# Kernel tuning notes

Hardware: AMD Instinct MI355X
Metric: run time of the kernel (lower is better)

The kernel has to match this reference:

```python
import jax, jax.numpy as jnp
import numpy as np

B, S, D, H = 4, 2048, 512, 8
HD = D // H


def rotate_half(t):
    half = t.shape[-1] // 2
    return jnp.concatenate([-t[..., half:], t[..., :half]], axis=-1)


def setup_inputs() -> dict:
    key = jax.random.key(0)
    ks = jax.random.split(key, 8)
    x = jax.random.normal(ks[0], (B, S, D), dtype=jnp.float32)
    # realistic rotary tables built from angles
    inv_freq = 1.0 / (10000.0 ** (jnp.arange(0, D // 2, dtype=jnp.float32) / (D // 2)))
    ang = jnp.arange(S, dtype=jnp.float32)[:, None] * inv_freq[None, :]  # [S, D/2]
    ang = jnp.concatenate([ang, ang], axis=-1)  # [S, D]
    cos_emb = jnp.cos(ang)[None]  # [1, S, D]
    sin_emb = jnp.sin(ang)[None]
    mask = jax.random.randint(ks[1], (B, S, S), 0, 2).astype(jnp.bool_)
    scale = 1.0 / np.sqrt(D)
    wq = jax.random.normal(ks[2], (D, D), dtype=jnp.float32) * scale
    wk = jax.random.normal(ks[3], (D, D), dtype=jnp.float32) * scale
    wv = jax.random.normal(ks[4], (D, D), dtype=jnp.float32) * scale
    wo = jax.random.normal(ks[5], (D, D), dtype=jnp.float32) * scale
    return {"x": x, "cos_emb": cos_emb, "sin_emb": sin_emb, "mask": mask,
            "wq": wq, "wk": wk, "wv": wv, "wo": wo}


def reference(x, cos_emb, sin_emb, mask, wq, wk, wv, wo):
    bsz, seqlen, dim = x.shape
    # projections (weights stored as [in, out])
    xq = x @ wq
    xk = x @ wk
    xv = x @ wv
    # RoPE applied over full dim before head split (as in original)
    xq = xq * cos_emb + rotate_half(xq) * sin_emb
    xk = xk * cos_emb + rotate_half(xk) * sin_emb
    # split heads: [B, H, S, HD]
    xq = xq.reshape(bsz, seqlen, H, HD).transpose(0, 2, 1, 3)
    xk = xk.reshape(bsz, seqlen, H, HD).transpose(0, 2, 1, 3)
    xv = xv.reshape(bsz, seqlen, H, HD).transpose(0, 2, 1, 3)
    scores = jnp.einsum('bhqd,bhkd->bhqk', xq, xk) / jnp.sqrt(jnp.float32(HD))
    scores = scores + (~mask)[:, None].astype(scores.dtype) * (-1e9)
    scores = jax.nn.softmax(scores.astype(jnp.float32), axis=-1).astype(xq.dtype)
    scores = scores * mask[:, None].astype(scores.dtype)
    out = jnp.einsum('bhqk,bhkd->bhqd', scores, xv)
    out = out.transpose(0, 2, 1, 3).reshape(bsz, seqlen, dim)
    return out @ wo
```

## Files before the change

kernel.cpp:

```cpp
#include <hip/hip_runtime.h>
#include <hip/hip_bf16.h>

typedef __bf16 bf16x8 __attribute__((ext_vector_type(8)));
typedef float f32x4 __attribute__((ext_vector_type(4)));
typedef short short8 __attribute__((ext_vector_type(8)));

#define MFMA16(a, b, c) __builtin_amdgcn_mfma_f32_16x16x32_bf16((a), (b), (c), 0, 0, 0)

static constexpr int S = 2048;
static constexpr int D = 512;
static constexpr int HD = 64;
static constexpr int KBLK = 64;
#define QSCALE 0.18033688011112042f

typedef __attribute__((address_space(1))) const unsigned int gu32;
typedef __attribute__((address_space(3))) unsigned int lu32;

__device__ __forceinline__ void gll16(const void* g, void* l) {
  __builtin_amdgcn_global_load_lds((gu32*)g, (lu32*)l, 16, 0, 0);
}

__device__ __forceinline__ unsigned short f2b(float f) {
  return __builtin_bit_cast(unsigned short, __float2bfloat16(f));
}
__device__ __forceinline__ float b2f(unsigned short u) {
  return __builtin_bit_cast(float, (unsigned)u << 16);
}

__global__ void maskbits_kernel(const int* __restrict__ m, unsigned long long* __restrict__ bits) {
  const int stride = 2048 * 256;
  const int lane0 = (threadIdx.x & 63) == 0;
  for (int gid = blockIdx.x * 256 + threadIdx.x; gid < 4 * 2048 * 2048; gid += stride) {
    unsigned long long w = __ballot(m[gid] != 0);
    if (lane0) bits[gid >> 6] = w;
  }
}

__global__ void cast_x_kernel(const float* __restrict__ x, unsigned short* __restrict__ xb) {
  int idx = blockIdx.x * 256 + threadIdx.x;
  float4 v = ((const float4*)x)[idx];
  ushort4 o;
  o.x = f2b(v.x); o.y = f2b(v.y); o.z = f2b(v.z); o.w = f2b(v.w);
  ((ushort4*)xb)[idx] = o;
}

__global__ void wtrans4_kernel(const float* __restrict__ wq, const float* __restrict__ wk,
                               const float* __restrict__ wv, const float* __restrict__ wo,
                               unsigned short* __restrict__ wqkvT, unsigned short* __restrict__ woT) {
  __shared__ float t[64][65];
  const int z = blockIdx.z;
  const float* w = (z == 0) ? wq : (z == 1) ? wk : (z == 2) ? wv : wo;
  unsigned short* dst = (z < 3) ? wqkvT + (size_t)z * 512 * 512 : woT;
  const int i0 = blockIdx.x * 64, o0 = blockIdx.y * 64;
  for (int it = 0; it < 16; ++it) {
    int idx = it * 256 + threadIdx.x;
    int ii = idx >> 6, oo = idx & 63;
    t[oo][ii] = w[(size_t)(i0 + ii) * 512 + o0 + oo];
  }
  __syncthreads();
  for (int it = 0; it < 16; ++it) {
    int idx = it * 256 + threadIdx.x;
    int oo = idx >> 6, ii = idx & 63;
    dst[(size_t)(o0 + oo) * 512 + i0 + ii] = f2b(t[oo][ii]);
  }
}

__global__ __launch_bounds__(256)
void gemm2(const unsigned short* __restrict__ A, const unsigned short* __restrict__ Bt,
           int M, int N, int K, float* __restrict__ Cf,
           unsigned short* __restrict__ qd, unsigned short* __restrict__ kd,
           unsigned short* __restrict__ vtd, int mode) {
  __shared__ alignas(16) unsigned char smem[36864];
  unsigned short (*lds)[2][4096] = (unsigned short (*)[2][4096])smem;
  const int tid = threadIdx.x;
  const int lane = tid & 63, l15 = lane & 15, lg = lane >> 4;
  const int wave = tid >> 6;
  const int m0 = blockIdx.x * 128, n0 = blockIdx.y * 128;
  const int wm = (wave >> 1) * 64, wn = (wave & 1) * 64;
  const int wbase = wave * 512;
  const int grow = tid >> 2, gcol = (tid & 3) * 8;
  f32x4 acc[4][4] = {};
  const int nt = K / 32;

#define GSTAGE(sb, kk)                                                              \
  do {                                                                              \
    gll16(&A[(size_t)(m0 + grow) * K + (kk) + gcol], &lds[sb][0][wbase]);           \
    gll16(&A[(size_t)(m0 + 64 + grow) * K + (kk) + gcol], &lds[sb][0][2048 + wbase]);\
    gll16(&Bt[(size_t)(n0 + grow) * K + (kk) + gcol], &lds[sb][1][wbase]);          \
    gll16(&Bt[(size_t)(n0 + 64 + grow) * K + (kk) + gcol], &lds[sb][1][2048 + wbase]);\
  } while (0)

  GSTAGE(0, 0);
  asm volatile("s_waitcnt vmcnt(0)" ::: "memory");
  __syncthreads();
  for (int t = 0; t < nt; ++t) {
    const int cur = t & 1;
    if (t + 1 < nt) GSTAGE(cur ^ 1, (t + 1) * 32);
    bf16x8 af[4], bfr[4];
#pragma unroll
    for (int i = 0; i < 4; ++i) {
      af[i]  = *(const bf16x8*)&lds[cur][0][(wm + i * 16 + l15) * 32 + lg * 8];
      bfr[i] = *(const bf16x8*)&lds[cur][1][(wn + i * 16 + l15) * 32 + lg * 8];
    }
    __builtin_amdgcn_s_setprio(1);
#pragma unroll
    for (int i = 0; i < 4; ++i)
#pragma unroll
      for (int j = 0; j < 4; ++j)
        acc[i][j] = MFMA16(af[i], bfr[j], acc[i][j]);
    __builtin_amdgcn_s_setprio(0);
    asm volatile("s_waitcnt vmcnt(0)" ::: "memory");
    __syncthreads();
  }
#undef GSTAGE

  if (mode == 0) {
#pragma unroll
    for (int i = 0; i < 4; ++i)
#pragma unroll
      for (int j = 0; j < 4; ++j)
#pragma unroll
        for (int r = 0; r < 4; ++r)
          Cf[(size_t)(m0 + wm + i * 16 + lg * 4 + r) * N + (n0 + wn + j * 16 + l15)] = acc[i][j][r];
  } else {
    const int sel = n0 >> 9;
    const int nb = (n0 & 511) + wn;
    if (sel < 2) {
      unsigned short* dst = (sel == 0) ? qd : kd;
#pragma unroll
      for (int i = 0; i < 4; ++i)
#pragma unroll
        for (int j = 0; j < 4; ++j)
#pragma unroll
          for (int r = 0; r < 4; ++r) {
            const int m = m0 + wm + i * 16 + lg * 4 + r;
            const int nn = nb + j * 16 + l15;
            dst[(((size_t)(m >> 11) * 8 + (nn >> 6)) * 2048 + (m & 2047)) * 64 + (nn & 63)] =
                f2b(acc[i][j][r]);
          }
    } else {
      unsigned short* tb = (unsigned short*)smem + wave * 4608;
#pragma unroll
      for (int i = 0; i < 4; ++i)
#pragma unroll
        for (int j = 0; j < 4; ++j) {
          ushort4 pk;
          pk.x = f2b(acc[i][j][0]); pk.y = f2b(acc[i][j][1]);
          pk.z = f2b(acc[i][j][2]); pk.w = f2b(acc[i][j][3]);
          *(ushort4*)&tb[(j * 16 + l15) * 72 + i * 16 + lg * 4] = pk;
        }
      const int b0 = m0 >> 11;
      const int s0 = (m0 & 2047) + wm;
      const int g = lane >> 3, c = lane & 7;
#pragma unroll
      for (int rr = 0; rr < 8; ++rr) {
        const int row = rr * 8 + g;
        const int nng = nb + row;
        uint4 v = *(const uint4*)&tb[row * 72 + c * 8];
        *(uint4*)&vtd[(((size_t)(b0 * 8) + (nng >> 6)) * 64 + (nng & 63)) * 2048 + s0 + c * 8] = v;
      }
    }
  }
}

__global__ void rope_pair_kernel(const unsigned short* __restrict__ qpre, const unsigned short* __restrict__ kpre,
                                 const float* __restrict__ cose, const float* __restrict__ sine,
                                 unsigned short* __restrict__ qb, unsigned short* __restrict__ kb) {
  const int idx = blockIdx.x * 256 + threadIdx.x;
  const int hd0 = (idx & 7) * 8;
  const int rr = idx >> 3;
  const int b = rr >> 13, h = (rr >> 11) & 3, s = rr & 2047;
  const size_t lo = ((size_t)(b * 8 + h) * 2048 + s) * 64 + hd0;
  const size_t hi = lo + (size_t)4 * 2048 * 64;
  const int d0 = h * 64 + hd0;
  short8 qlo = *(const short8*)&qpre[lo];
  short8 qhi = *(const short8*)&qpre[hi];
  short8 klo = *(const short8*)&kpre[lo];
  short8 khi = *(const short8*)&kpre[hi];
  float4 c0 = *(const float4*)&cose[(size_t)s * 512 + d0];
  float4 c1 = *(const float4*)&cose[(size_t)s * 512 + d0 + 4];
  float4 s0 = *(const float4*)&sine[(size_t)s * 512 + d0];
  float4 s1 = *(const float4*)&sine[(size_t)s * 512 + d0 + 4];
  float cc[8] = {c0.x, c0.y, c0.z, c0.w, c1.x, c1.y, c1.z, c1.w};
  float ss[8] = {s0.x, s0.y, s0.z, s0.w, s1.x, s1.y, s1.z, s1.w};
  short8 qolo, qohi, kolo, kohi;
#pragma unroll
  for (int j = 0; j < 8; ++j) {
    float ql = b2f((unsigned short)qlo[j]), qh = b2f((unsigned short)qhi[j]);
    float kl = b2f((unsigned short)klo[j]), kh = b2f((unsigned short)khi[j]);
    qolo[j] = (short)f2b((ql * cc[j] - qh * ss[j]) * QSCALE);
    qohi[j] = (short)f2b((qh * cc[j] + ql * ss[j]) * QSCALE);
    kolo[j] = (short)f2b(kl * cc[j] - kh * ss[j]);
    kohi[j] = (short)f2b(kh * cc[j] + kl * ss[j]);
  }
  *(short8*)&qb[lo] = qolo;
  *(short8*)&qb[hi] = qohi;
  *(short8*)&kb[lo] = kolo;
  *(short8*)&kb[hi] = kohi;
}

__global__ __launch_bounds__(512)
void flash_kernel(const unsigned short* __restrict__ qb, const unsigned short* __restrict__ kb,
                  const unsigned short* __restrict__ vtb, const unsigned long long* __restrict__ mbits,
                  float* __restrict__ op0, float* __restrict__ op1,
                  float* __restrict__ ls0, float* __restrict__ ls1) {
  __shared__ alignas(16) unsigned short kv[2][2][4096];
  __shared__ alignas(16) f32x4 btab[16];
  const int tid = threadIdx.x;
  const int wave = tid >> 6, lane = tid & 63;
  const int l15 = lane & 15, lg = lane >> 4;
  const int swz = (l15 & 7) << 4;
  const int wgid = blockIdx.x;
  const int slot = wgid >> 3;
  const int bh = (wgid & 7) * 4 + (slot & 3);
  const int rest = slot >> 2;
  const int kh = rest & 1;
  const int q0 = (rest >> 1) * 128 + wave * 16;
  const int b = bh >> 3, h = bh & 7;
  const int kbase = kh * 1024;
  const unsigned short* Q = qb + ((size_t)bh * S + q0) * HD;
  const unsigned short* Kp = kb + (size_t)bh * S * HD;
  const unsigned short* Vt = vtb + (size_t)bh * HD * S;
  const unsigned long long* Mrow = mbits + ((size_t)b * S + q0 + l15) * (S / 64) + kh * 16;
  float* opart = kh ? op1 : op0;
  float* lsum = kh ? ls1 : ls0;

  const int srow = tid >> 3;
  const int scol = ((tid & 7) ^ (srow & 7)) * 8;
  const int ksrow = ((srow & 15) >> 2) * 8 + ((srow >> 4) & 1) * 4 + (srow & 3) + (srow >> 5) * 32;
  const int wbase = wave * 512;

  if (tid < 16) {
    f32x4 e;
    e[0] = (tid & 1) ? 0.f : -300.f;
    e[1] = (tid & 2) ? 0.f : -300.f;
    e[2] = (tid & 4) ? 0.f : -300.f;
    e[3] = (tid & 8) ? 0.f : -300.f;
    btab[tid] = e;
  }

  bf16x8 qf0 = *(const bf16x8*)&Q[l15 * HD + lg * 8];
  bf16x8 qf1 = *(const bf16x8*)&Q[l15 * HD + 32 + lg * 8];
  f32x4 o[4] = {};
  float lpart = 0.f;
  const int lgs8 = lg * 8;

  unsigned long long wA = Mrow[0];
  gll16(&Kp[(size_t)(kbase + ksrow) * HD + scol], &kv[0][0][wbase]);
  gll16(&Vt[(size_t)srow * S + kbase + scol], &kv[0][1][wbase]);
  asm volatile("s_waitcnt vmcnt(0) lgkmcnt(0)" ::: "memory");
  __syncthreads();

  for (int t = 0; t < 16; ++t) {
    const int cur = t & 1;
    unsigned long long wB = 0;
    if (t + 1 < 16) {
      const int kn = kbase + (t + 1) * KBLK;
      gll16(&Kp[(size_t)(kn + ksrow) * HD + scol], &kv[cur ^ 1][0][wbase]);
      gll16(&Vt[(size_t)srow * S + kn + scol], &kv[cur ^ 1][1][wbase]);
      wB = Mrow[t + 1];
    }
    const char* kbp = (const char*)&kv[cur][0][0];
    const char* vbp = (const char*)&kv[cur][1][0];

    f32x4 sc[4] = {};
    __builtin_amdgcn_s_setprio(1);
#pragma unroll
    for (int n = 0; n < 4; ++n) {
      const int cb = (n * 16 + l15) * 128 + ((lg * 16) ^ swz);
      bf16x8 kf0 = *(const bf16x8*)(kbp + cb);
      bf16x8 kf1 = *(const bf16x8*)(kbp + (cb ^ 64));
      sc[n] = MFMA16(kf0, qf0, sc[n]);
      sc[n] = MFMA16(kf1, qf1, sc[n]);
    }
    __builtin_amdgcn_s_setprio(0);

    f32x4 pv[4];
    {
      const f32x4 b0 = btab[(unsigned)(wA >> (lgs8 + 0)) & 15u];
      const f32x4 b1 = btab[(unsigned)(wA >> (lgs8 + 4)) & 15u];
      const f32x4 b2 = btab[(unsigned)(wA >> (lgs8 + 32)) & 15u];
      const f32x4 b3 = btab[(unsigned)(wA >> (lgs8 + 36)) & 15u];
#pragma unroll
      for (int r = 0; r < 4; ++r) {
        pv[0][r] = __builtin_amdgcn_exp2f(sc[0][r] + b0[r]);
        pv[1][r] = __builtin_amdgcn_exp2f(sc[1][r] + b1[r]);
        pv[2][r] = __builtin_amdgcn_exp2f(sc[2][r] + b2[r]);
        pv[3][r] = __builtin_amdgcn_exp2f(sc[3][r] + b3[r]);
      }
    }
    f32x4 s4 = (pv[0] + pv[1]) + (pv[2] + pv[3]);
    lpart += (s4[0] + s4[1]) + (s4[2] + s4[3]);

    bf16x8 pf0, pf1;
#pragma unroll
    for (int j = 0; j < 4; ++j) {
      pf0[j]     = (__bf16)pv[0][j];
      pf0[j + 4] = (__bf16)pv[1][j];
      pf1[j]     = (__bf16)pv[2][j];
      pf1[j + 4] = (__bf16)pv[3][j];
    }

    __builtin_amdgcn_s_setprio(1);
#pragma unroll
    for (int n = 0; n < 4; ++n) {
      const int cb = (n * 16 + l15) * 128 + ((lg * 16) ^ swz);
      bf16x8 vf0 = *(const bf16x8*)(vbp + cb);
      bf16x8 vf1 = *(const bf16x8*)(vbp + (cb ^ 64));
      o[n] = MFMA16(pf0, vf0, o[n]);
      o[n] = MFMA16(pf1, vf1, o[n]);
    }
    __builtin_amdgcn_s_setprio(0);

    asm volatile("s_waitcnt vmcnt(0)" ::: "memory");
    __syncthreads();
    wA = wB;
  }

  lpart += __shfl_xor(lpart, 16);
  lpart += __shfl_xor(lpart, 32);
  if (lg == 0) lsum[(size_t)bh * S + q0 + l15] = lpart;
#pragma unroll
  for (int r = 0; r < 4; ++r)
#pragma unroll
    for (int n = 0; n < 4; ++n)
      opart[((size_t)(b * S + q0 + lg * 4 + r)) * D + h * HD + n * 16 + l15] = o[n][r];
}

__global__ __launch_bounds__(256)
void gemm_fused(const float* __restrict__ op0, const float* __restrict__ op1,
                const float* __restrict__ ls0, const float* __restrict__ ls1,
                const unsigned short* __restrict__ Bt, float* __restrict__ C) {
  __shared__ alignas(16) unsigned short ldsA[2][2048];
  __shared__ alignas(16) unsigned short ldsB[2][4096];
  __shared__ float invt[512];
  const int tid = threadIdx.x;
  const int lane = tid & 63, l15 = lane & 15, lg = lane >> 4;
  const int wave = tid >> 6;
  const int m0 = blockIdx.x * 64, n0 = blockIdx.y * 128;
  const int wm = (wave >> 1) * 32, wn = (wave & 1) * 64;
  const int wbase = wave * 512;
  const int grow = tid >> 2, gcol = (tid & 3) * 8;
  const size_t abase = (size_t)(m0 + (tid >> 2)) * 512 + (tid & 3) * 8;
  f32x4 acc[2][4] = {};

  for (int e = tid; e < 512; e += 256) {
    const int row = e >> 3, hh = e & 7;
    const int m = m0 + row;
    const size_t li = ((size_t)((m >> 11) * 8 + hh)) * 2048 + (m & 2047);
    const float l = ls0[li] + ls1[li];
    invt[e] = (l > 0.f) ? 1.f / l : 0.f;
  }

#define BSTAGE(sb, kk)                                                               \
  do {                                                                               \
    gll16(&Bt[(size_t)(n0 + grow) * 512 + (kk) + gcol], &ldsB[sb][wbase]);           \
    gll16(&Bt[(size_t)(n0 + 64 + grow) * 512 + (kk) + gcol], &ldsB[sb][2048 + wbase]);\
  } while (0)

  float4 a0, a1, p0, p1;
#define ALOAD(kk)                                          \
  do {                                                     \
    a0 = *(const float4*)&op0[abase + (kk)];               \
    a1 = *(const float4*)&op0[abase + (kk) + 4];           \
    p0 = *(const float4*)&op1[abase + (kk)];               \
    p1 = *(const float4*)&op1[abase + (kk) + 4];           \
  } while (0)

#define AWRITE(sb, kk)                                                       \
  do {                                                                       \
    const float inv = invt[((tid >> 2) << 3) | ((kk) >> 6)];                 \
    short8 pk;                                                               \
    pk[0] = (short)f2b((a0.x + p0.x) * inv);                                 \
    pk[1] = (short)f2b((a0.y + p0.y) * inv);                                 \
    pk[2] = (short)f2b((a0.z + p0.z) * inv);                                 \
    pk[3] = (short)f2b((a0.w + p0.w) * inv);                                 \
    pk[4] = (short)f2b((a1.x + p1.x) * inv);                                 \
    pk[5] = (short)f2b((a1.y + p1.y) * inv);                                 \
    pk[6] = (short)f2b((a1.z + p1.z) * inv);                                 \
    pk[7] = (short)f2b((a1.w + p1.w) * inv);                                 \
    *(short8*)&ldsA[sb][(tid >> 2) * 32 + (tid & 3) * 8] = pk;               \
  } while (0)

  ALOAD(0);
  BSTAGE(0, 0);
  __syncthreads();
  AWRITE(0, 0);
  __syncthreads();

  for (int t = 0; t < 16; ++t) {
    const int cur = t & 1;
    const bool have = (t + 1 < 16);
    if (have) { ALOAD((t + 1) * 32); BSTAGE(cur ^ 1, (t + 1) * 32); }
    bf16x8 af[2], bfr[4];
#pragma unroll
    for (int i = 0; i < 2; ++i)
      af[i] = *(const bf16x8*)&ldsA[cur][(wm + i * 16 + l15) * 32 + lg * 8];
#pragma unroll
    for (int j = 0; j < 4; ++j)
      bfr[j] = *(const bf16x8*)&ldsB[cur][(wn + j * 16 + l15) * 32 + lg * 8];
    __builtin_amdgcn_s_setprio(1);
#pragma unroll
    for (int i = 0; i < 2; ++i)
#pragma unroll
      for (int j = 0; j < 4; ++j)
        acc[i][j] = MFMA16(af[i], bfr[j], acc[i][j]);
    __builtin_amdgcn_s_setprio(0);
    asm volatile("s_waitcnt vmcnt(0)" ::: "memory");
    __syncthreads();
    if (have) AWRITE(cur ^ 1, (t + 1) * 32);
    __syncthreads();
  }
#undef BSTAGE
#undef ALOAD
#undef AWRITE

#pragma unroll
  for (int i = 0; i < 2; ++i)
#pragma unroll
    for (int j = 0; j < 4; ++j)
#pragma unroll
      for (int r = 0; r < 4; ++r)
        C[(size_t)(m0 + wm + i * 16 + lg * 4 + r) * 512 + (n0 + wn + j * 16 + l15)] = acc[i][j][r];
}

extern "C" void kernel_launch(void* const* d_in, const int* in_sizes, int n_in,
                              void* d_out, int out_size, void* d_ws, size_t ws_size,
                              hipStream_t stream) {
  const float* x = (const float*)d_in[0];
  const float* cose = (const float*)d_in[1];
  const float* sine = (const float*)d_in[2];
  const int* mask = (const int*)d_in[3];
  const float* wq = (const float*)d_in[4];
  const float* wk = (const float*)d_in[5];
  const float* wv = (const float*)d_in[6];
  const float* wo = (const float*)d_in[7];
  float* out = (float*)d_out;
  char* ws = (char*)d_ws;

  unsigned short* xb    = (unsigned short*)(ws);
  unsigned short* wqkvT = (unsigned short*)(ws + 8388608);
  unsigned short* woT   = (unsigned short*)(ws + 9961472);
  unsigned short* qpre  = (unsigned short*)(ws + 10485760);
  unsigned short* kpre  = (unsigned short*)(ws + 18874368);
  unsigned short* qbh   = (unsigned short*)(ws + 35651584);
  unsigned short* kbh   = (unsigned short*)(ws + 44040192);
  unsigned short* vtb   = (unsigned short*)(ws + 52428800);
  unsigned long long* mbits = (unsigned long long*)(ws + 60817408);
  float* op0 = (float*)(ws + 10485760);
  float* op1 = (float*)(ws + 62914560);
  float* ls0 = (float*)(ws + 79691776);
  float* ls1 = (float*)(ws + 79953920);

  maskbits_kernel<<<2048, 256, 0, stream>>>(mask, mbits);
  cast_x_kernel<<<4096, 256, 0, stream>>>(x, xb);
  wtrans4_kernel<<<dim3(8, 8, 4), 256, 0, stream>>>(wq, wk, wv, wo, wqkvT, woT);
  gemm2<<<dim3(64, 12), 256, 0, stream>>>(xb, wqkvT, 8192, 1536, 512, nullptr, qpre, kpre, vtb, 1);
  rope_pair_kernel<<<1024, 256, 0, stream>>>(qpre, kpre, cose, sine, qbh, kbh);
  flash_kernel<<<1024, 512, 0, stream>>>(qbh, kbh, vtb, mbits, op0, op1, ls0, ls1);
  gemm_fused<<<dim3(128, 4), 256, 0, stream>>>(op0, op1, ls0, ls1, woT, out);
}
```

Baseline: 123.0 us.

## Process two query tiles per flash block and merge prep kernels into one launch

The flash kernel now has each wave handle two 16-row query tiles, 128 rows apart. Each K/V tile loaded into LDS is reused for twice as many queries, and the grid is halved to 512 blocks. Score computation and softmax are interleaved per 16-column chunk to keep register use in check. Mask bit-packing, the x cast and the weight transposes are merged into one prep kernel to save launches. The risks are higher register pressure and fewer workgroups, which gives less parallelism across CUs.

```diff
diff --git a/kernel.cpp b/kernel.cpp
--- a/kernel.cpp
+++ b/kernel.cpp
@@ -27,41 +27,44 @@
   return __builtin_bit_cast(float, (unsigned)u << 16);
 }
 
-__global__ void maskbits_kernel(const int* __restrict__ m, unsigned long long* __restrict__ bits) {
-  const int stride = 2048 * 256;
-  const int lane0 = (threadIdx.x & 63) == 0;
-  for (int gid = blockIdx.x * 256 + threadIdx.x; gid < 4 * 2048 * 2048; gid += stride) {
-    unsigned long long w = __ballot(m[gid] != 0);
-    if (lane0) bits[gid >> 6] = w;
-  }
-}
-
-__global__ void cast_x_kernel(const float* __restrict__ x, unsigned short* __restrict__ xb) {
-  int idx = blockIdx.x * 256 + threadIdx.x;
-  float4 v = ((const float4*)x)[idx];
-  ushort4 o;
-  o.x = f2b(v.x); o.y = f2b(v.y); o.z = f2b(v.z); o.w = f2b(v.w);
-  ((ushort4*)xb)[idx] = o;
-}
-
-__global__ void wtrans4_kernel(const float* __restrict__ wq, const float* __restrict__ wk,
-                               const float* __restrict__ wv, const float* __restrict__ wo,
-                               unsigned short* __restrict__ wqkvT, unsigned short* __restrict__ woT) {
+__global__ void prep_kernel(const float* __restrict__ x, unsigned short* __restrict__ xb,
+                            const int* __restrict__ m, unsigned long long* __restrict__ bits,
+                            const float* __restrict__ wq, const float* __restrict__ wk,
+                            const float* __restrict__ wv, const float* __restrict__ wo,
+                            unsigned short* __restrict__ wqkvT, unsigned short* __restrict__ woT) {
   __shared__ float t[64][65];
-  const int z = blockIdx.z;
-  const float* w = (z == 0) ? wq : (z == 1) ? wk : (z == 2) ? wv : wo;
-  unsigned short* dst = (z < 3) ? wqkvT + (size_t)z * 512 * 512 : woT;
-  const int i0 = blockIdx.x * 64, o0 = blockIdx.y * 64;
-  for (int it = 0; it < 16; ++it) {
-    int idx = it * 256 + threadIdx.x;
-    int ii = idx >> 6, oo = idx & 63;
-    t[oo][ii] = w[(size_t)(i0 + ii) * 512 + o0 + oo];
-  }
-  __syncthreads();
-  for (int it = 0; it < 16; ++it) {
-    int idx = it * 256 + threadIdx.x;
-    int oo = idx >> 6, ii = idx & 63;
-    dst[(size_t)(o0 + oo) * 512 + i0 + ii] = f2b(t[oo][ii]);
+  const int blk = blockIdx.x;
+  const int tid = threadIdx.x;
+  if (blk < 4096) {
+    int idx = blk * 256 + tid;
+    float4 v = ((const float4*)x)[idx];
+    ushort4 o;
+    o.x = f2b(v.x); o.y = f2b(v.y); o.z = f2b(v.z); o.w = f2b(v.w);
+    ((ushort4*)xb)[idx] = o;
+  } else if (blk < 6144) {
+    const int stride = 2048 * 256;
+    const int lane0 = (tid & 63) == 0;
+    for (int gid = (blk - 4096) * 256 + tid; gid < 4 * 2048 * 2048; gid += stride) {
+      unsigned long long w = __ballot(m[gid] != 0);
+      if (lane0) bits[gid >> 6] = w;
+    }
+  } else {
+    const int tt = blk - 6144;
+    const int z = tt >> 6, r = tt & 63;
+    const float* w = (z == 0) ? wq : (z == 1) ? wk : (z == 2) ? wv : wo;
+    unsigned short* dst = (z < 3) ? wqkvT + (size_t)z * 512 * 512 : woT;
+    const int i0 = (r & 7) * 64, o0 = (r >> 3) * 64;
+    for (int it = 0; it < 16; ++it) {
+      int idx = it * 256 + tid;
+      int ii = idx >> 6, oo = idx & 63;
+      t[oo][ii] = w[(size_t)(i0 + ii) * 512 + o0 + oo];
+    }
+    __syncthreads();
+    for (int it = 0; it < 16; ++it) {
+      int idx = it * 256 + tid;
+      int oo = idx >> 6, ii = idx & 63;
+      dst[(size_t)(o0 + oo) * 512 + i0 + ii] = f2b(t[oo][ii]);
+    }
   }
 }
 
@@ -215,13 +218,14 @@
   const int bh = (wgid & 7) * 4 + (slot & 3);
   const int rest = slot >> 2;
   const int kh = rest & 1;
-  const int q0 = (rest >> 1) * 128 + wave * 16;
+  const int q0 = (rest >> 1) * 256 + wave * 16;
   const int b = bh >> 3, h = bh & 7;
   const int kbase = kh * 1024;
   const unsigned short* Q = qb + ((size_t)bh * S + q0) * HD;
   const unsigned short* Kp = kb + (size_t)bh * S * HD;
   const unsigned short* Vt = vtb + (size_t)bh * HD * S;
-  const unsigned long long* Mrow = mbits + ((size_t)b * S + q0 + l15) * (S / 64) + kh * 16;
+  const unsigned long long* MrowA = mbits + ((size_t)b * S + q0 + l15) * (S / 64) + kh * 16;
+  const unsigned long long* MrowB = MrowA + (size_t)128 * (S / 64);
   float* opart = kh ? op1 : op0;
   float* lsum = kh ? ls1 : ls0;
 
@@ -239,13 +243,15 @@
     btab[tid] = e;
   }
 
-  bf16x8 qf0 = *(const bf16x8*)&Q[l15 * HD + lg * 8];
-  bf16x8 qf1 = *(const bf16x8*)&Q[l15 * HD + 32 + lg * 8];
-  f32x4 o[4] = {};
-  float lpart = 0.f;
+  bf16x8 qf0a = *(const bf16x8*)&Q[l15 * HD + lg * 8];
+  bf16x8 qf1a = *(const bf16x8*)&Q[l15 * HD + 32 + lg * 8];
+  bf16x8 qf0b = *(const bf16x8*)&Q[(128 + l15) * HD + lg * 8];
+  bf16x8 qf1b = *(const bf16x8*)&Q[(128 + l15) * HD + 32 + lg * 8];
+  f32x4 oa[4] = {}, ob[4] = {};
+  float lpa = 0.f, lpb = 0.f;
   const int lgs8 = lg * 8;
 
-  unsigned long long wA = Mrow[0];
+  unsigned long long wAa = MrowA[0], wAb = MrowB[0];
   gll16(&Kp[(size_t)(kbase + ksrow) * HD + scol], &kv[0][0][wbase]);
   gll16(&Vt[(size_t)srow * S + kbase + scol], &kv[0][1][wbase]);
   asm volatile("s_waitcnt vmcnt(0) lgkmcnt(0)" ::: "memory");
@@ -253,52 +259,49 @@
 
   for (int t = 0; t < 16; ++t) {
     const int cur = t & 1;
-    unsigned long long wB = 0;
+    unsigned long long wBa = 0, wBb = 0;
     if (t + 1 < 16) {
       const int kn = kbase + (t + 1) * KBLK;
       gll16(&Kp[(size_t)(kn + ksrow) * HD + scol], &kv[cur ^ 1][0][wbase]);
       gll16(&Vt[(size_t)srow * S + kn + scol], &kv[cur ^ 1][1][wbase]);
-      wB = Mrow[t + 1];
+      wBa = MrowA[t + 1];
+      wBb = MrowB[t + 1];
     }
     const char* kbp = (const char*)&kv[cur][0][0];
     const char* vbp = (const char*)&kv[cur][1][0];
 
-    f32x4 sc[4] = {};
-    __builtin_amdgcn_s_setprio(1);
+    bf16x8 pf0a, pf1a, pf0b, pf1b;
 #pragma unroll
     for (int n = 0; n < 4; ++n) {
       const int cb = (n * 16 + l15) * 128 + ((lg * 16) ^ swz);
       bf16x8 kf0 = *(const bf16x8*)(kbp + cb);
       bf16x8 kf1 = *(const bf16x8*)(kbp + (cb ^ 64));
-      sc[n] = MFMA16(kf0, qf0, sc[n]);
-      sc[n] = MFMA16(kf1, qf1, sc[n]);
-    }
-    __builtin_amdgcn_s_setprio(0);
-
-    f32x4 pv[4];
-    {
-      const f32x4 b0 = btab[(unsigned)(wA >> (lgs8 + 0)) & 15u];
-      const f32x4 b1 = btab[(unsigned)(wA >> (lgs8 + 4)) & 15u];
-      const f32x4 b2 = btab[(unsigned)(wA >> (lgs8 + 32)) & 15u];
-      const f32x4 b3 = btab[(unsigned)(wA >> (lgs8 + 36)) & 15u];
+      f32x4 scA = {}, scB = {};
+      __builtin_amdgcn_s_setprio(1);
+      scA = MFMA16(kf0, qf0a, scA);
+      scA = MFMA16(kf1, qf1a, scA);
+      scB = MFMA16(kf0, qf0b, scB);
+      scB = MFMA16(kf1, qf1b, scB);
+      __builtin_amdgcn_s_setprio(0);
+      const int sh = (n == 0) ? 0 : (n == 1) ? 4 : (n == 2) ? 32 : 36;
+      const f32x4 ba = btab[(unsigned)(wAa >> (lgs8 + sh)) & 15u];
+      const f32x4 bb = btab[(unsigned)(wAb >> (lgs8 + sh)) & 15u];
+      f32x4 pa, pb;
 #pragma unroll
       for (int r = 0; r < 4; ++r) {
-        pv[0][r] = __builtin_amdgcn_exp2f(sc[0][r] + b0[r]);
-        pv[1][r] = __builtin_amdgcn_exp2f(sc[1][r] + b1[r]);
-        pv[2][r] = __builtin_amdgcn_exp2f(sc[2][r] + b2[r]);
-        pv[3][r] = __builtin_amdgcn_exp2f(sc[3][r] + b3[r]);
+        pa[r] = __builtin_amdgcn_exp2f(scA[r] + ba[r]);
+        pb[r] = __builtin_amdgcn_exp2f(scB[r] + bb[r]);
       }
-    }
-    f32x4 s4 = (pv[0] + pv[1]) + (pv[2] + pv[3]);
-    lpart += (s4[0] + s4[1]) + (s4[2] + s4[3]);
-
-    bf16x8 pf0, pf1;
-#pragma unroll
-    for (int j = 0; j < 4; ++j) {
-      pf0[j]     = (__bf16)pv[0][j];
-      pf0[j + 4] = (__bf16)pv[1][j];
-      pf1[j]     = (__bf16)pv[2][j];
-      pf1[j + 4] = (__bf16)pv[3][j];
+      lpa += (pa[0] + pa[1]) + (pa[2] + pa[3]);
+      lpb += (pb[0] + pb[1]) + (pb[2] + pb[3]);
+      bf16x8& dsta = (n < 2) ? pf0a : pf1a;
+      bf16x8& dstb = (n < 2) ? pf0b : pf1b;
+      const int jo = (n & 1) * 4;
+#pragma unroll
+      for (int j = 0; j < 4; ++j) {
+        dsta[jo + j] = (__bf16)pa[j];
+        dstb[jo + j] = (__bf16)pb[j];
+      }
     }
 
     __builtin_amdgcn_s_setprio(1);
@@ -307,24 +310,34 @@
       const int cb = (n * 16 + l15) * 128 + ((lg * 16) ^ swz);
       bf16x8 vf0 = *(const bf16x8*)(vbp + cb);
       bf16x8 vf1 = *(const bf16x8*)(vbp + (cb ^ 64));
-      o[n] = MFMA16(pf0, vf0, o[n]);
-      o[n] = MFMA16(pf1, vf1, o[n]);
+      oa[n] = MFMA16(pf0a, vf0, oa[n]);
+      oa[n] = MFMA16(pf1a, vf1, oa[n]);
+      ob[n] = MFMA16(pf0b, vf0, ob[n]);
+      ob[n] = MFMA16(pf1b, vf1, ob[n]);
     }
     __builtin_amdgcn_s_setprio(0);
 
     asm volatile("s_waitcnt vmcnt(0)" ::: "memory");
     __syncthreads();
-    wA = wB;
-  }
-
-  lpart += __shfl_xor(lpart, 16);
-  lpart += __shfl_xor(lpart, 32);
-  if (lg == 0) lsum[(size_t)bh * S + q0 + l15] = lpart;
+    wAa = wBa;
+    wAb = wBb;
+  }
+
+  lpa += __shfl_xor(lpa, 16);
+  lpa += __shfl_xor(lpa, 32);
+  lpb += __shfl_xor(lpb, 16);
+  lpb += __shfl_xor(lpb, 32);
+  if (lg == 0) {
+    lsum[(size_t)bh * S + q0 + l15] = lpa;
+    lsum[(size_t)bh * S + q0 + 128 + l15] = lpb;
+  }
 #pragma unroll
   for (int r = 0; r < 4; ++r)
 #pragma unroll
-    for (int n = 0; n < 4; ++n)
-      opart[((size_t)(b * S + q0 + lg * 4 + r)) * D + h * HD + n * 16 + l15] = o[n][r];
+    for (int n = 0; n < 4; ++n) {
+      opart[((size_t)(b * S + q0 + lg * 4 + r)) * D + h * HD + n * 16 + l15] = oa[n][r];
+      opart[((size_t)(b * S + q0 + 128 + lg * 4 + r)) * D + h * HD + n * 16 + l15] = ob[n][r];
+    }
 }
 
 __global__ __launch_bounds__(256)
@@ -452,11 +465,9 @@
   float* ls0 = (float*)(ws + 79691776);
   float* ls1 = (float*)(ws + 79953920);
 
-  maskbits_kernel<<<2048, 256, 0, stream>>>(mask, mbits);
-  cast_x_kernel<<<4096, 256, 0, stream>>>(x, xb);
-  wtrans4_kernel<<<dim3(8, 8, 4), 256, 0, stream>>>(wq, wk, wv, wo, wqkvT, woT);
+  prep_kernel<<<6400, 256, 0, stream>>>(x, xb, mask, mbits, wq, wk, wv, wo, wqkvT, woT);
   gemm2<<<dim3(64, 12), 256, 0, stream>>>(xb, wqkvT, 8192, 1536, 512, nullptr, qpre, kpre, vtb, 1);
   rope_pair_kernel<<<1024, 256, 0, stream>>>(qpre, kpre, cose, sine, qbh, kbh);
-  flash_kernel<<<1024, 512, 0, stream>>>(qbh, kbh, vtb, mbits, op0, op1, ls0, ls1);
+  flash_kernel<<<512, 512, 0, stream>>>(qbh, kbh, vtb, mbits, op0, op1, ls0, ls1);
   gemm_fused<<<dim3(128, 4), 256, 0, stream>>>(op0, op1, ls0, ls1, woT, out);
 }
```

New measurement: 115.9 us, median of 2. -5.8%, faster.
